# Optimization experiments

Hardware: AMD Instinct MI355X
Metric: run time of the kernel (lower is better)

Reference implementation:

```python
import jax, jax.numpy as jnp
import numpy as np

B, T, F, H = 256, 512, 64, 128


def _uniform(key, shape, stdv):
    return jax.random.uniform(key, shape, jnp.float32, -stdv, stdv)


def setup_inputs() -> dict:
    key = jax.random.key(0)
    ks = jax.random.split(key, 24)
    values = jax.random.normal(ks[0], (B, T, F), jnp.float32)
    masks = (jax.random.uniform(ks[1], (B, T, F)) < 0.8).astype(jnp.float32)
    deltas = jax.random.uniform(ks[2], (B, T, F), jnp.float32)
    labels = (jax.random.uniform(ks[3], (B, 1)) < 0.5).astype(jnp.float32)
    is_train = (jax.random.uniform(ks[4], (B, 1)) < 0.8).astype(jnp.float32)
    sH = 1.0 / np.sqrt(H)
    sF = 1.0 / np.sqrt(F)
    # temp_decay_h: Linear F -> H (stdv = 1/sqrt(out) per reset_parameters)
    W_dh = _uniform(ks[5], (H, F), sH); b_dh = _uniform(ks[6], (H,), sH)
    # temp_decay_x: diag F -> F
    W_dx = _uniform(ks[7], (F, F), sF); b_dx = _uniform(ks[8], (F,), sF)
    # hist_reg: Linear H -> F (torch Linear stdv = 1/sqrt(in))
    W_hr = _uniform(ks[9], (F, H), sH); b_hr = _uniform(ks[10], (F,), sH)
    # feat_reg: F -> F with zeroed diagonal mask
    W_fr = _uniform(ks[11], (F, F), sF); b_fr = _uniform(ks[12], (F,), sF)
    # weight_combine: Linear 2F -> F
    s2F = 1.0 / np.sqrt(2 * F)
    W_wc = _uniform(ks[13], (F, 2 * F), s2F); b_wc = _uniform(ks[14], (F,), s2F)
    # LSTMCell(2F, H): torch init uniform(-1/sqrt(H), 1/sqrt(H)), gate order i,f,g,o
    W_ih = _uniform(ks[15], (4 * H, 2 * F), sH); b_ih = _uniform(ks[16], (4 * H,), sH)
    W_hh = _uniform(ks[17], (4 * H, H), sH); b_hh = _uniform(ks[18], (4 * H,), sH)
    # out: Linear H -> 1
    W_out = _uniform(ks[19], (1, H), sH); b_out = _uniform(ks[20], (1,), sH)
    return dict(values=values, masks=masks, deltas=deltas, labels=labels, is_train=is_train,
                W_dh=W_dh, b_dh=b_dh, W_dx=W_dx, b_dx=b_dx, W_hr=W_hr, b_hr=b_hr,
                W_fr=W_fr, b_fr=b_fr, W_wc=W_wc, b_wc=b_wc,
                W_ih=W_ih, b_ih=b_ih, W_hh=W_hh, b_hh=b_hh, W_out=W_out, b_out=b_out)


def _forward(values, masks, deltas, labels, is_train,
             W_dh, b_dh, W_dx, b_dx, W_hr, b_hr, W_fr, b_fr, W_wc, b_wc,
             W_ih, b_ih, W_hh, b_hh, W_out, b_out):
    eps = 1e-5
    w_dx_diag = jnp.diagonal(W_dx)            # diag mask: W * I
    W_fr_m = W_fr * (1.0 - jnp.eye(F, dtype=W_fr.dtype))  # zero diagonal

    def step(carry, xs):
        h, c, x_loss = carry
        x, m, d = xs                           # each [B, F]
        gamma_h = jnp.exp(-jax.nn.relu(d @ W_dh.T + b_dh))   # [B, H]
        gamma_x = jnp.exp(-jax.nn.relu(d * w_dx_diag + b_dx))  # [B, F]
        h = h * gamma_h
        x_h = h @ W_hr.T + b_hr                # [B, F]
        msum = jnp.sum(m) + eps
        x_loss = x_loss + jnp.sum(jnp.abs(x - x_h) * m) / msum
        x_c = m * x + (1.0 - m) * x_h
        z_h = x_c @ W_fr_m.T + b_fr
        x_loss = x_loss + jnp.sum(jnp.abs(x - z_h) * m) / msum
        alpha = jnp.concatenate([gamma_x, m], axis=1) @ W_wc.T + b_wc
        c_h = alpha * z_h + (1.0 - alpha) * x_h
        x_loss = x_loss + jnp.sum(jnp.abs(x - c_h) * m) / msum
        c_c = m * x + (1.0 - m) * c_h
        inp = jnp.concatenate([c_c, m], axis=1)   # [B, 2F]
        gates = inp @ W_ih.T + b_ih + h @ W_hh.T + b_hh  # [B, 4H]
        i, f, g, o = jnp.split(gates, 4, axis=1)
        c = jax.nn.sigmoid(f) * c + jax.nn.sigmoid(i) * jnp.tanh(g)
        h = jax.nn.sigmoid(o) * jnp.tanh(c)
        return (h, c, x_loss), c_c

    h0 = jnp.zeros((values.shape[0], H), values.dtype)
    c0 = jnp.zeros((values.shape[0], H), values.dtype)
    xs = (jnp.swapaxes(values, 0, 1), jnp.swapaxes(masks, 0, 1), jnp.swapaxes(deltas, 0, 1))
    (h, c, x_loss), imps = jax.lax.scan(step, (h0, c0, jnp.float32(0.0)), xs)
    imputations = jnp.swapaxes(imps, 0, 1)     # [B, T, F]
    y_h = h @ W_out.T + b_out                  # [B, 1] logits
    # stable BCE with logits (matches torch reference formula)
    max_val = jnp.maximum(-y_h, 0.0)
    y_l = y_h - y_h * labels + max_val + jnp.log(jnp.exp(-max_val) + jnp.exp(-y_h - max_val))
    y_loss = jnp.sum(y_l * is_train) / (jnp.sum(is_train) + eps)
    loss = x_loss / T + y_loss * 0.3
    predictions = jax.nn.sigmoid(y_h)
    return loss, predictions, imputations


def reference(values, masks, deltas, labels, is_train,
              W_dh, b_dh, W_dx, b_dx, W_hr, b_hr, W_fr, b_fr, W_wc, b_wc,
              W_ih, b_ih, W_hh, b_hh, W_out, b_out):
    return _forward(values, masks, deltas, labels, is_train,
                    W_dh, b_dh, W_dx, b_dx, W_hr, b_hr, W_fr, b_fr, W_wc, b_wc,
                    W_ih, b_ih, W_hh, b_hh, W_out, b_out)
```

## Files before the change

### kernel.cpp

```cpp
#include <hip/hip_runtime.h>
#include <hip/hip_fp16.h>


#define NBATCH 256
#define NT 512
#define NF 64
#define NH 128

#define WHH_OFF   0u
#define WIH_OFF   131072u
#define WHR_OFF   262144u
#define WFR_OFF   278528u
#define INVMS_OFF 286720u
#define ISTR_OFF  288768u
#define GH_OFF    294912u
#define AL_OFF    33849344u

typedef _Float16 half2_t __attribute__((ext_vector_type(2)));

__device__ __forceinline__ unsigned pack2(float a, float b) {
    __half2 h = __floats2half2_rn(a, b);
    return __builtin_bit_cast(unsigned, h);
}

__device__ __forceinline__ float dot2f(unsigned w, unsigned a, float acc) {
#if __has_builtin(__builtin_amdgcn_fdot2)
    return __builtin_amdgcn_fdot2(__builtin_bit_cast(half2_t, w),
                                  __builtin_bit_cast(half2_t, a), acc, false);
#else
    float2 wf = __half22float2(__builtin_bit_cast(__half2, w));
    float2 af = __half22float2(__builtin_bit_cast(__half2, a));
    return acc + wf.x * af.x + wf.y * af.y;
#endif
}

__device__ __forceinline__ float sigm(float x) { return 1.f / (1.f + __expf(-x)); }
__device__ __forceinline__ float tanh_fast(float x) { return 1.f - 2.f / (__expf(2.f * x) + 1.f); }

__device__ __forceinline__ float quad_add_x1(float v) {
    int r = __builtin_amdgcn_update_dpp(0, __builtin_bit_cast(int, v),
                                        0xB1 , 0xF, 0xF, true);
    return v + __builtin_bit_cast(float, r);
}
__device__ __forceinline__ float quad_add_x2(float v) {
    int r = __builtin_amdgcn_update_dpp(0, __builtin_bit_cast(int, v),
                                        0x4E , 0xF, 0xF, true);
    return v + __builtin_bit_cast(float, r);
}

#define KEEP4(u) asm volatile("" : "+v"(u.x), "+v"(u.y), "+v"(u.z), "+v"(u.w))

__global__ __launch_bounds__(256) void prep_w(const float* __restrict__ Whh,
                                              const float* __restrict__ Wih,
                                              const float* __restrict__ Whr,
                                              const float* __restrict__ Wfr,
                                              unsigned* __restrict__ wsu) {
    int o = blockIdx.x * 256 + threadIdx.x;
    float v0, v1;
    if (o < 32768) {
        int c = o & 3, r = (o >> 2) & 511, cb = o >> 11;
        int col = 8 * cb + 2 * c;
        v0 = Whh[r * 128 + col]; v1 = Whh[r * 128 + col + 1];
    } else if (o < 65536) {
        int o2 = o - 32768;
        int c = o2 & 3, r = (o2 >> 2) & 511, cb = o2 >> 11;
        int col = 8 * cb + 2 * c;
        v0 = Wih[r * 128 + col]; v1 = Wih[r * 128 + col + 1];
    } else if (o < 69632) {
        int o3 = o - 65536;
        int c = o3 & 3, f = (o3 >> 2) & 63, cb = o3 >> 8;
        int col = 8 * cb + 2 * c;
        v0 = Whr[f * 128 + col]; v1 = Whr[f * 128 + col + 1];
    } else if (o < 71680) {
        int o4 = o - 69632;
        int c = o4 & 3, f = (o4 >> 2) & 63, cb = o4 >> 8;
        int col = 8 * cb + 2 * c;
        v0 = (col == f) ? 0.f : Wfr[f * 64 + col];
        v1 = (col + 1 == f) ? 0.f : Wfr[f * 64 + col + 1];
    } else {
        return;
    }
    wsu[o] = pack2(v0, v1);
}

__global__ __launch_bounds__(256) void prep_msum(const float* __restrict__ masks,
                                                 const float* __restrict__ is_train,
                                                 float* __restrict__ invms,
                                                 float* __restrict__ inv_istr,
                                                 float* __restrict__ d_out0) {
    __shared__ float red[256];
    int tid = threadIdx.x;
    int t = blockIdx.x;
    if (t < NT) {
        int f = tid & 63, br = tid >> 6;
        float s = 0.f;
        for (int i = 0; i < 64; i++) {
            int b = br + i * 4;
            s += masks[((size_t)b * NT + t) * NF + f];
        }
        red[tid] = s;
        __syncthreads();
        for (int off = 128; off > 0; off >>= 1) {
            if (tid < off) red[tid] += red[tid + off];
            __syncthreads();
        }
        if (tid == 0) invms[t] = 1.f / (red[0] + 1e-5f);
    } else {
        red[tid] = is_train[tid];
        __syncthreads();
        for (int off = 128; off > 0; off >>= 1) {
            if (tid < off) red[tid] += red[tid + off];
            __syncthreads();
        }
        if (tid == 0) {
            *inv_istr = 1.f / (red[0] + 1e-5f);
            *d_out0 = 0.f;
        }
    }
}

__global__ __launch_bounds__(256) void ga_kernel(const float* __restrict__ deltas,
                                                 const float* __restrict__ masks,
                                                 const float* __restrict__ Wdh,
                                                 const float* __restrict__ bdh,
                                                 const float* __restrict__ Wdx,
                                                 const float* __restrict__ bdx,
                                                 const float* __restrict__ Wwc,
                                                 const float* __restrict__ bwc,
                                                 __half* __restrict__ gh_all,
                                                 __half* __restrict__ al_all) {
    __shared__ unsigned wdhpk[32 * 128];
    __shared__ unsigned wwcpk[64 * 64];
    __shared__ float sbdh[128], sbdx[64], swdx[64], sbwc[64];
    __shared__ float dbuf[64];
    __shared__ __align__(16) unsigned dpk[32], gxpk[32], mpk2[32];
    int tid = threadIdx.x;

    for (int o = tid; o < 4096; o += 256) {
        int j = o & 127, k2 = o >> 7;
        wdhpk[o] = pack2(Wdh[j * 64 + 2 * k2], Wdh[j * 64 + 2 * k2 + 1]);
    }
    for (int o = tid; o < 4096; o += 256) {
        int f = o & 63, k2 = o >> 6;
        wwcpk[o] = pack2(Wwc[f * 128 + 2 * k2], Wwc[f * 128 + 2 * k2 + 1]);
    }
    if (tid < 128) sbdh[tid] = bdh[tid];
    if (tid < 64) {
        sbdx[tid] = bdx[tid];
        swdx[tid] = Wdx[tid * 65];
        sbwc[tid] = bwc[tid];
    }
    __syncthreads();

    for (int i = 0; i < 32; i++) {
        int p = blockIdx.x * 32 + i;
        if (tid < 32) {
            float2 dv = ((const float2*)(deltas + (size_t)p * NF))[tid];
            dbuf[2 * tid] = dv.x; dbuf[2 * tid + 1] = dv.y;
            dpk[tid] = pack2(dv.x, dv.y);
        } else if (tid < 64) {
            int q = tid - 32;
            float2 mv = ((const float2*)(masks + (size_t)p * NF))[q];
            mpk2[q] = pack2(mv.x, mv.y);
        }
        __syncthreads();
        if (tid < 64) {
            float gx = __expf(-fmaxf(dbuf[tid] * swdx[tid] + sbdx[tid], 0.f));
            float oth = __shfl_xor(gx, 1);
            if (!(tid & 1)) gxpk[tid >> 1] = pack2(gx, oth);
        }
        __syncthreads();
        if (tid < 128) {
            float a0 = sbdh[tid], a1 = 0.f;
            #pragma unroll
            for (int k8 = 0; k8 < 8; k8++) {
                uint4 dp = *(const uint4*)&dpk[4 * k8];
                a0 = dot2f(wdhpk[(4 * k8 + 0) * 128 + tid], dp.x, a0);
                a1 = dot2f(wdhpk[(4 * k8 + 1) * 128 + tid], dp.y, a1);
                a0 = dot2f(wdhpk[(4 * k8 + 2) * 128 + tid], dp.z, a0);
                a1 = dot2f(wdhpk[(4 * k8 + 3) * 128 + tid], dp.w, a1);
            }
            gh_all[(size_t)p * NH + tid] = __float2half(__expf(-fmaxf(a0 + a1, 0.f)));
        } else if (tid < 192) {
            int f = tid - 128;
            float a0 = sbwc[f], a1 = 0.f;
            #pragma unroll
            for (int k8 = 0; k8 < 8; k8++) {
                uint4 gp = *(const uint4*)&gxpk[4 * k8];
                a0 = dot2f(wwcpk[(4 * k8 + 0) * 64 + f], gp.x, a0);
                a1 = dot2f(wwcpk[(4 * k8 + 1) * 64 + f], gp.y, a1);
                a0 = dot2f(wwcpk[(4 * k8 + 2) * 64 + f], gp.z, a0);
                a1 = dot2f(wwcpk[(4 * k8 + 3) * 64 + f], gp.w, a1);
            }
            #pragma unroll
            for (int k8 = 0; k8 < 8; k8++) {
                uint4 mp = *(const uint4*)&mpk2[4 * k8];
                a0 = dot2f(wwcpk[(32 + 4 * k8 + 0) * 64 + f], mp.x, a0);
                a1 = dot2f(wwcpk[(32 + 4 * k8 + 1) * 64 + f], mp.y, a1);
                a0 = dot2f(wwcpk[(32 + 4 * k8 + 2) * 64 + f], mp.z, a0);
                a1 = dot2f(wwcpk[(32 + 4 * k8 + 3) * 64 + f], mp.w, a1);
            }
            al_all[(size_t)p * NF + f] = __float2half(a0 + a1);
        }
        __syncthreads();
    }
}

__global__ __launch_bounds__(512, 1) void main_kernel(
    const float* __restrict__ values, const float* __restrict__ masks,
    const float* __restrict__ labels, const float* __restrict__ is_train,
    const float* __restrict__ b_hr, const float* __restrict__ b_fr,
    const float* __restrict__ b_ih, const float* __restrict__ b_hh,
    const float* __restrict__ W_out, const float* __restrict__ b_out,
    const uint4* __restrict__ whh_ws, const uint4* __restrict__ wih_ws,
    const uint4* __restrict__ whr_ws, const uint4* __restrict__ wfr_ws,
    const float* __restrict__ invms, const float* __restrict__ inv_istr,
    const __half* __restrict__ gh_all, const __half* __restrict__ al_all,
    float* __restrict__ d_out) {
    __shared__ uint4 wm[512 * 9];
    __shared__ uint4 wfr4[8 * 64];
    __shared__ float sbhr[64], sbfr[64];
    __shared__ __align__(16) __half hph[128];
    __shared__ float xp[512];
    __shared__ float xbuf4[4][64], albuf4[4][64], mbuf4[4][64];
    __shared__ __align__(16) unsigned mpk4[4][32];
    __shared__ __align__(16) __half xcph[64], ccph[64];
    __shared__ __align__(16) unsigned ghpk4[4][64];
    __shared__ float invt4[4];
    __shared__ float hfin[128];

    const int tid = threadIdx.x;
    const int b = blockIdx.x;
    const int s = tid & 3;
    const int cq = tid >> 2;
    const int kg = tid >> 6;
    const int fl = tid & 63;

    uint4 whh_q[16];
    uint4 wihc_q[8];
    float bg4[4];
    #pragma unroll
    for (int g = 0; g < 4; g++) {
        int r = g * 128 + cq;
        #pragma unroll
        for (int j = 0; j < 4; j++) whh_q[g * 4 + j] = whh_ws[(4 * s + j) * 512 + r];
        #pragma unroll
        for (int j = 0; j < 2; j++)
            wihc_q[g * 2 + j] = wih_ws[(2 * s + j) * 512 + r];
        bg4[g] = b_ih[r] + b_hh[r];
    }
    uint4 whr_pa = whr_ws[(2 * kg) * 64 + fl];
    uint4 whr_pb = whr_ws[(2 * kg + 1) * 64 + fl];
    for (int o = tid; o < 4096; o += 512) {
        int r = o & 511, c = o >> 9;
        wm[r * 9 + c] = wih_ws[(8 + c) * 512 + r];
    }
    wfr4[tid] = wfr_ws[tid];
    if (tid < 64) { sbhr[tid] = b_hr[tid]; sbfr[tid] = b_fr[tid]; }
    if (tid < 128) hph[tid] = __float2half(0.f);

    const float* vp = values + (size_t)b * NT * NF;
    const float* mp = masks + (size_t)b * NT * NF;
    const __half* alp = al_all + (size_t)b * NT * NF;
    const unsigned* ghu = (const unsigned*)(gh_all + (size_t)b * NT * NH);
    float* imp = d_out + 257 + (size_t)b * NT * NF;

    float creg = 0.f;
    float lloss = 0.f;
    float hacc4[4] = {0.f, 0.f, 0.f, 0.f};
    float macc4[4] = {0.f, 0.f, 0.f, 0.f};
    float ccb0 = 0.f, ccb1 = 0.f, ccb2 = 0.f, ccb3 = 0.f;

    float xr4[4] = {0.f, 0.f, 0.f, 0.f};
    __half ar4[4] = {};
    float ir4[4] = {0.f, 0.f, 0.f, 0.f};
    float2 mr4[4] = {};
    unsigned gr4[4] = {0u, 0u, 0u, 0u};

    if (tid >= 256 && tid < 320) {
        int q = tid - 256;
        #pragma unroll
        for (int u = 0; u < 4; u++) {
            xr4[u] = vp[u * NF + q];
            ar4[u] = alp[u * NF + q];
        }
        if (q == 0) {
            #pragma unroll
            for (int u = 0; u < 4; u++) ir4[u] = invms[u];
        }
    } else if (tid >= 320 && tid < 352) {
        int q = tid - 320;
        #pragma unroll
        for (int u = 0; u < 4; u++) mr4[u] = ((const float2*)(mp + u * NF))[q];
    } else if (tid >= 352 && tid < 416) {
        int q = tid - 352;
        #pragma unroll
        for (int u = 0; u < 4; u++) gr4[u] = ghu[(size_t)(u + 1) * 64 + q];
    }
    __syncthreads();

    const int wmr = cq * 9;

    for (int tb = 0; tb < NT; tb += 4) {
        #pragma unroll
        for (int i = 0; i < 16; i++) { KEEP4(whh_q[i]); }
        #pragma unroll
        for (int i = 0; i < 8; i++) { KEEP4(wihc_q[i]); }
        KEEP4(whr_pa); KEEP4(whr_pb);

        #pragma unroll
        for (int j = 0; j < 4; j++) {
            const int t = tb + j;
            if (j == 0) {
                if (tid >= 256 && tid < 320) {
                    int q = tid - 256;
                    #pragma unroll
                    for (int u = 0; u < 4; u++) {
                        xbuf4[u][q] = xr4[u];
                        albuf4[u][q] = __half2float(ar4[u]);
                    }
                    if (q == 0) {
                        #pragma unroll
                        for (int u = 0; u < 4; u++) invt4[u] = ir4[u];
                    }
                    #pragma unroll
                    for (int u = 0; u < 4; u++) {
                        int tn = tb + 4 + u; if (tn > NT - 1) tn = NT - 1;
                        xr4[u] = vp[tn * NF + q];
                        ar4[u] = alp[tn * NF + q];
                    }
                    if (q == 0) {
                        #pragma unroll
                        for (int u = 0; u < 4; u++) {
                            int tn = tb + 4 + u; if (tn > NT - 1) tn = NT - 1;
                            ir4[u] = invms[tn];
                        }
                    }
                } else if (tid >= 320 && tid < 352) {
                    int q = tid - 320;
                    #pragma unroll
                    for (int u = 0; u < 4; u++) {
                        mbuf4[u][2 * q] = mr4[u].x; mbuf4[u][2 * q + 1] = mr4[u].y;
                        mpk4[u][q] = pack2(mr4[u].x, mr4[u].y);
                    }
                    #pragma unroll
                    for (int u = 0; u < 4; u++) {
                        int tn = tb + 4 + u; if (tn > NT - 1) tn = NT - 1;
                        mr4[u] = ((const float2*)(mp + tn * NF))[q];
                    }
                } else if (tid >= 352 && tid < 416) {
                    int q = tid - 352;
                    #pragma unroll
                    for (int u = 0; u < 4; u++) ghpk4[u][q] = gr4[u];
                    #pragma unroll
                    for (int u = 0; u < 4; u++) {
                        int tg = tb + 5 + u; if (tg > NT - 1) tg = NT - 1;
                        gr4[u] = ghu[(size_t)tg * 64 + q];
                    }
                }
            }
            #pragma unroll
            for (int g = 0; g < 4; g++) {
                float u0 = 0.f, u1 = 0.f;
                #pragma unroll
                for (int jj = 0; jj < 4; jj++) {
                    uint4 hq = *(const uint4*)&hph[32 * s + 8 * jj];
                    uint4 w = whh_q[g * 4 + jj];
                    u0 = dot2f(w.x, hq.x, u0); u1 = dot2f(w.y, hq.y, u1);
                    u0 = dot2f(w.z, hq.z, u0); u1 = dot2f(w.w, hq.w, u1);
                }
                hacc4[g] = u0 + u1;
            }
            {
                uint4 hpa = *(const uint4*)&hph[16 * kg];
                uint4 hpb = *(const uint4*)&hph[16 * kg + 8];
                float p0, p1;
                p0 = dot2f(whr_pa.x, hpa.x, 0.f); p1 = dot2f(whr_pa.y, hpa.y, 0.f);
                p0 = dot2f(whr_pa.z, hpa.z, p0);  p1 = dot2f(whr_pa.w, hpa.w, p1);
                p0 = dot2f(whr_pb.x, hpb.x, p0);  p1 = dot2f(whr_pb.y, hpb.y, p1);
                p0 = dot2f(whr_pb.z, hpb.z, p0);  p1 = dot2f(whr_pb.w, hpb.w, p1);
                xp[tid] = p0 + p1;
            }
            __syncthreads();

            if (tid < 64) {
                __builtin_amdgcn_s_setprio(1);
                float xh = sbhr[fl];
                #pragma unroll
                for (int g8 = 0; g8 < 8; g8++) xh += xp[g8 * 64 + fl];
                float xv = xbuf4[j][fl], mv = mbuf4[j][fl];
                float av = albuf4[j][fl], it = invt4[j];
                float xc = mv * xv + (1.f - mv) * xh;
                xcph[fl] = __float2half(xc);
                float b0 = sbfr[fl], b1 = 0.f;
                #pragma unroll
                for (int k4 = 0; k4 < 8; k4++) {
                    uint4 w = wfr4[k4 * 64 + fl];
                    uint4 xq = *(const uint4*)&xcph[8 * k4];
                    b0 = dot2f(w.x, xq.x, b0); b1 = dot2f(w.y, xq.y, b1);
                    b0 = dot2f(w.z, xq.z, b0); b1 = dot2f(w.w, xq.w, b1);
                }
                float zh = b0 + b1;
                float ch = av * zh + (1.f - av) * xh;
                float cc = mv * xv + (1.f - mv) * ch;
                if (j == 0) ccb0 = cc; else if (j == 1) ccb1 = cc;
                else if (j == 2) ccb2 = cc; else ccb3 = cc;
                lloss += (fabsf(xv - xh) + fabsf(xv - zh) + fabsf(xv - ch)) * mv * it;
                ccph[fl] = __float2half(cc);
                if (j == 3) {
                    imp[(tb + 0) * NF + fl] = ccb0;
                    imp[(tb + 1) * NF + fl] = ccb1;
                    imp[(tb + 2) * NF + fl] = ccb2;
                    imp[(tb + 3) * NF + fl] = ccb3;
                }
                __builtin_amdgcn_s_setprio(0);
            } else {
                uint4 mq0 = *(const uint4*)&mpk4[j][8 * s];
                uint4 mq1 = *(const uint4*)&mpk4[j][8 * s + 4];
                #pragma unroll
                for (int g = 0; g < 4; g++) {
                    uint4 wa = wm[(g * 128 + cq) * 9 + 2 * s];
                    uint4 wb = wm[(g * 128 + cq) * 9 + 2 * s + 1];
                    float u0 = dot2f(wa.x, mq0.x, 0.f), u1 = dot2f(wa.y, mq0.y, 0.f);
                    u0 = dot2f(wa.z, mq0.z, u0); u1 = dot2f(wa.w, mq0.w, u1);
                    u0 = dot2f(wb.x, mq1.x, u0); u1 = dot2f(wb.y, mq1.y, u1);
                    u0 = dot2f(wb.z, mq1.z, u0); u1 = dot2f(wb.w, mq1.w, u1);
                    macc4[g] = u0 + u1;
                }
            }
            __syncthreads();

            {
                if (tid < 64) {
                    uint4 mq0 = *(const uint4*)&mpk4[j][8 * s];
                    uint4 mq1 = *(const uint4*)&mpk4[j][8 * s + 4];
                    #pragma unroll
                    for (int g = 0; g < 4; g++) {
                        uint4 wa = wm[(g * 128 + cq) * 9 + 2 * s];
                        uint4 wb = wm[(g * 128 + cq) * 9 + 2 * s + 1];
                        float u0 = dot2f(wa.x, mq0.x, 0.f), u1 = dot2f(wa.y, mq0.y, 0.f);
                        u0 = dot2f(wa.z, mq0.z, u0); u1 = dot2f(wa.w, mq0.w, u1);
                        u0 = dot2f(wb.x, mq1.x, u0); u1 = dot2f(wb.y, mq1.y, u1);
                        u0 = dot2f(wb.z, mq1.z, u0); u1 = dot2f(wb.w, mq1.w, u1);
                        macc4[g] = u0 + u1;
                    }
                }
                uint4 cq0 = *(const uint4*)&ccph[16 * s];
                uint4 cq1 = *(const uint4*)&ccph[16 * s + 8];
                float gate[4];
                #pragma unroll
                for (int g = 0; g < 4; g++) {
                    uint4 wa = wihc_q[g * 2], wb = wihc_q[g * 2 + 1];
                    float u0 = dot2f(wa.x, cq0.x, 0.f), u1 = dot2f(wa.y, cq0.y, 0.f);
                    u0 = dot2f(wa.z, cq0.z, u0); u1 = dot2f(wa.w, cq0.w, u1);
                    u0 = dot2f(wb.x, cq1.x, u0); u1 = dot2f(wb.y, cq1.y, u1);
                    u0 = dot2f(wb.z, cq1.z, u0); u1 = dot2f(wb.w, cq1.w, u1);
                    float v = hacc4[g] + macc4[g] + (u0 + u1);
                    v = quad_add_x1(v);
                    v = quad_add_x2(v);
                    gate[g] = v + bg4[g];
                }
                float cn = sigm(gate[1]) * creg + sigm(gate[0]) * tanh_fast(gate[2]);
                creg = cn;
                float hn = sigm(gate[3]) * tanh_fast(cn);
                float gm = __half2float(((const __half*)&ghpk4[j][0])[cq]);
                float hd = hn * gm;
                if (s == 0) hph[cq] = __float2half(hd);
                if (t == NT - 1 && s == 0) hfin[cq] = hn;
            }
            __syncthreads();
        }
    }

    if (tid < 64) {
        float ll = lloss;
        float yp = hfin[tid] * W_out[tid] + hfin[64 + tid] * W_out[64 + tid];
        #pragma unroll
        for (int off = 32; off > 0; off >>= 1) {
            ll += __shfl_down(ll, off);
            yp += __shfl_down(yp, off);
        }
        if (tid == 0) {
            float yh = yp + b_out[0];
            d_out[1 + b] = 1.f / (1.f + expf(-yh));
            float lab = labels[b], istr = is_train[b];
            float maxv = fmaxf(-yh, 0.f);
            float yl = yh - yh * lab + maxv + logf(expf(-maxv) + expf(-yh - maxv));
            atomicAdd(d_out, ll * (1.f / (float)NT) + 0.3f * yl * istr * (*inv_istr));
        }
    }
}

extern "C" void kernel_launch(void* const* d_in, const int* in_sizes, int n_in,
                              void* d_out, int out_size, void* d_ws, size_t ws_size,
                              hipStream_t stream) {
    const float* values = (const float*)d_in[0];
    const float* masks = (const float*)d_in[1];
    const float* deltas = (const float*)d_in[2];
    const float* labels = (const float*)d_in[3];
    const float* is_train = (const float*)d_in[4];
    const float* W_dh = (const float*)d_in[5];
    const float* b_dh = (const float*)d_in[6];
    const float* W_dx = (const float*)d_in[7];
    const float* b_dx = (const float*)d_in[8];
    const float* W_hr = (const float*)d_in[9];
    const float* b_hr = (const float*)d_in[10];
    const float* W_fr = (const float*)d_in[11];
    const float* b_fr = (const float*)d_in[12];
    const float* W_wc = (const float*)d_in[13];
    const float* b_wc = (const float*)d_in[14];
    const float* W_ih = (const float*)d_in[15];
    const float* b_ih = (const float*)d_in[16];
    const float* W_hh = (const float*)d_in[17];
    const float* b_hh = (const float*)d_in[18];
    const float* W_out = (const float*)d_in[19];
    const float* b_out = (const float*)d_in[20];

    char* ws = (char*)d_ws;
    unsigned* wsu = (unsigned*)d_ws;
    const uint4* whh_ws = (const uint4*)(ws + WHH_OFF);
    const uint4* wih_ws = (const uint4*)(ws + WIH_OFF);
    const uint4* whr_ws = (const uint4*)(ws + WHR_OFF);
    const uint4* wfr_ws = (const uint4*)(ws + WFR_OFF);
    float* invms = (float*)(ws + INVMS_OFF);
    float* inv_istr = (float*)(ws + ISTR_OFF);
    __half* gh_all = (__half*)(ws + GH_OFF);
    __half* al_all = (__half*)(ws + AL_OFF);
    float* out_f = (float*)d_out;

    prep_w<<<280, 256, 0, stream>>>(W_hh, W_ih, W_hr, W_fr, wsu);
    prep_msum<<<513, 256, 0, stream>>>(masks, is_train, invms, inv_istr, out_f);
    ga_kernel<<<4096, 256, 0, stream>>>(deltas, masks, W_dh, b_dh, W_dx, b_dx,
                                        W_wc, b_wc, gh_all, al_all);
    main_kernel<<<NBATCH, 512, 0, stream>>>(values, masks, labels, is_train,
                                            b_hr, b_fr, b_ih, b_hh, W_out, b_out,
                                            whh_ws, wih_ws, whr_ws, wfr_ws,
                                            invms, inv_istr, gh_all, al_all, out_f);
}
```

Baseline: 1.240 ms.

## Precompute mask-input LSTM gate contributions in parallel pre-pass kernel

Moves the W_ih·mask term of the LSTM gates (plus the biases) out of the sequential main kernel into the parallel ga_kernel. There it is written as a half-precision gate tensor that main_kernel prefetches per timestep. This takes dot products off the recurrent critical path and frees one LDS weight block. In exchange it adds about 128 MB of extra global writes and reads, and the path only runs when the workspace is large enough.

```diff
diff --git a/kernel.cpp b/kernel.cpp
--- a/kernel.cpp
+++ b/kernel.cpp
@@ -15,6 +15,8 @@
 #define ISTR_OFF  288768u
 #define GH_OFF    294912u
 #define AL_OFF    33849344u
+#define GM4_OFF   50626560u
+#define GM4_BYTES 134217728u
 
 typedef _Float16 half2_t __attribute__((ext_vector_type(2)));
 
@@ -127,8 +129,13 @@
                                                  const float* __restrict__ bdx,
                                                  const float* __restrict__ Wwc,
                                                  const float* __restrict__ bwc,
+                                                 const float* __restrict__ bih,
+                                                 const float* __restrict__ bhh,
+                                                 const uint4* __restrict__ wih_ws,
                                                  __half* __restrict__ gh_all,
-                                                 __half* __restrict__ al_all) {
+                                                 __half* __restrict__ al_all,
+                                                 __half* __restrict__ gm4_all,
+                                                 int do_gm) {
     __shared__ unsigned wdhpk[32 * 128];
     __shared__ unsigned wwcpk[64 * 64];
     __shared__ float sbdh[128], sbdx[64], swdx[64], sbwc[64];
@@ -149,6 +156,17 @@
         sbdx[tid] = bdx[tid];
         swdx[tid] = Wdx[tid * 65];
         sbwc[tid] = bwc[tid];
+    }
+    uint4 wmr0[8], wmr1[8];
+    float bgr0 = 0.f, bgr1 = 0.f;
+    if (do_gm) {
+        #pragma unroll
+        for (int c = 0; c < 8; c++) {
+            wmr0[c] = wih_ws[(8 + c) * 512 + tid];
+            wmr1[c] = wih_ws[(8 + c) * 512 + tid + 256];
+        }
+        bgr0 = bih[tid] + bhh[tid];
+        bgr1 = bih[tid + 256] + bhh[tid + 256];
     }
     __syncthreads();
 
@@ -202,6 +220,21 @@
             }
             al_all[(size_t)p * NF + f] = __float2half(a0 + a1);
         }
+        if (do_gm) {
+            float a0 = bgr0, a1 = 0.f, b0 = bgr1, b1 = 0.f;
+            #pragma unroll
+            for (int k8 = 0; k8 < 8; k8++) {
+                uint4 mp = *(const uint4*)&mpk2[4 * k8];
+                a0 = dot2f(wmr0[k8].x, mp.x, a0); a1 = dot2f(wmr0[k8].y, mp.y, a1);
+                a0 = dot2f(wmr0[k8].z, mp.z, a0); a1 = dot2f(wmr0[k8].w, mp.w, a1);
+                b0 = dot2f(wmr1[k8].x, mp.x, b0); b1 = dot2f(wmr1[k8].y, mp.y, b1);
+                b0 = dot2f(wmr1[k8].z, mp.z, b0); b1 = dot2f(wmr1[k8].w, mp.w, b1);
+            }
+            int cell = tid & 127;
+            int g0 = tid >> 7;
+            gm4_all[(size_t)p * 512 + cell * 4 + g0] = __float2half(a0 + a1);
+            gm4_all[(size_t)p * 512 + cell * 4 + g0 + 2] = __float2half(b0 + b1);
+        }
         __syncthreads();
     }
 }
@@ -216,6 +249,7 @@
     const uint4* __restrict__ whr_ws, const uint4* __restrict__ wfr_ws,
     const float* __restrict__ invms, const float* __restrict__ inv_istr,
     const __half* __restrict__ gh_all, const __half* __restrict__ al_all,
+    const __half* __restrict__ gm4_all,
     float* __restrict__ d_out) {
     __shared__ uint4 wm[512 * 9];
     __shared__ uint4 wfr4[8 * 64];
@@ -235,6 +269,7 @@
     const int cq = tid >> 2;
     const int kg = tid >> 6;
     const int fl = tid & 63;
+    const bool use_gm = (gm4_all != nullptr);
 
     uint4 whh_q[16];
     uint4 wihc_q[8];
@@ -251,9 +286,11 @@
     }
     uint4 whr_pa = whr_ws[(2 * kg) * 64 + fl];
     uint4 whr_pb = whr_ws[(2 * kg + 1) * 64 + fl];
-    for (int o = tid; o < 4096; o += 512) {
-        int r = o & 511, c = o >> 9;
-        wm[r * 9 + c] = wih_ws[(8 + c) * 512 + r];
+    if (!use_gm) {
+        for (int o = tid; o < 4096; o += 512) {
+            int r = o & 511, c = o >> 9;
+            wm[r * 9 + c] = wih_ws[(8 + c) * 512 + r];
+        }
     }
     wfr4[tid] = wfr_ws[tid];
     if (tid < 64) { sbhr[tid] = b_hr[tid]; sbfr[tid] = b_fr[tid]; }
@@ -263,6 +300,7 @@
     const float* mp = masks + (size_t)b * NT * NF;
     const __half* alp = al_all + (size_t)b * NT * NF;
     const unsigned* ghu = (const unsigned*)(gh_all + (size_t)b * NT * NH);
+    const __half* gmp = use_gm ? (gm4_all + (size_t)b * NT * 512) : nullptr;
     float* imp = d_out + 257 + (size_t)b * NT * NF;
 
     float creg = 0.f;
@@ -276,6 +314,7 @@
     float ir4[4] = {0.f, 0.f, 0.f, 0.f};
     float2 mr4[4] = {};
     unsigned gr4[4] = {0u, 0u, 0u, 0u};
+    uint2 gmr4[4] = {}; uint2 gmc[4] = {};
 
     if (tid >= 256 && tid < 320) {
         int q = tid - 256;
@@ -297,9 +336,12 @@
         #pragma unroll
         for (int u = 0; u < 4; u++) gr4[u] = ghu[(size_t)(u + 1) * 64 + q];
     }
+    if (use_gm) {
+        #pragma unroll
+        for (int u = 0; u < 4; u++)
+            gmr4[u] = *(const uint2*)(gmp + (size_t)u * 512 + cq * 4);
+    }
     __syncthreads();
-
-    const int wmr = cq * 9;
 
     for (int tb = 0; tb < NT; tb += 4) {
         #pragma unroll
@@ -341,7 +383,7 @@
                     #pragma unroll
                     for (int u = 0; u < 4; u++) {
                         mbuf4[u][2 * q] = mr4[u].x; mbuf4[u][2 * q + 1] = mr4[u].y;
-                        mpk4[u][q] = pack2(mr4[u].x, mr4[u].y);
+                        if (!use_gm) mpk4[u][q] = pack2(mr4[u].x, mr4[u].y);
                     }
                     #pragma unroll
                     for (int u = 0; u < 4; u++) {
@@ -356,6 +398,15 @@
                     for (int u = 0; u < 4; u++) {
                         int tg = tb + 5 + u; if (tg > NT - 1) tg = NT - 1;
                         gr4[u] = ghu[(size_t)tg * 64 + q];
+                    }
+                }
+                if (use_gm) {
+                    #pragma unroll
+                    for (int u = 0; u < 4; u++) gmc[u] = gmr4[u];
+                    #pragma unroll
+                    for (int u = 0; u < 4; u++) {
+                        int tn = tb + 4 + u; if (tn > NT - 1) tn = NT - 1;
+                        gmr4[u] = *(const uint2*)(gmp + (size_t)tn * 512 + cq * 4);
                     }
                 }
             }
@@ -414,7 +465,7 @@
                     imp[(tb + 3) * NF + fl] = ccb3;
                 }
                 __builtin_amdgcn_s_setprio(0);
-            } else {
+            } else if (!use_gm) {
                 uint4 mq0 = *(const uint4*)&mpk4[j][8 * s];
                 uint4 mq1 = *(const uint4*)&mpk4[j][8 * s + 4];
                 #pragma unroll
@@ -431,7 +482,7 @@
             __syncthreads();
 
             {
-                if (tid < 64) {
+                if (!use_gm && tid < 64) {
                     uint4 mq0 = *(const uint4*)&mpk4[j][8 * s];
                     uint4 mq1 = *(const uint4*)&mpk4[j][8 * s + 4];
                     #pragma unroll
@@ -444,6 +495,12 @@
                         u0 = dot2f(wb.z, mq1.z, u0); u1 = dot2f(wb.w, mq1.w, u1);
                         macc4[g] = u0 + u1;
                     }
+                }
+                float gmf[4] = {bg4[0], bg4[1], bg4[2], bg4[3]};
+                if (use_gm) {
+                    float2 f01 = __half22float2(__builtin_bit_cast(__half2, gmc[j].x));
+                    float2 f23 = __half22float2(__builtin_bit_cast(__half2, gmc[j].y));
+                    gmf[0] = f01.x; gmf[1] = f01.y; gmf[2] = f23.x; gmf[3] = f23.y;
                 }
                 uint4 cq0 = *(const uint4*)&ccph[16 * s];
                 uint4 cq1 = *(const uint4*)&ccph[16 * s + 8];
@@ -455,10 +512,11 @@
                     u0 = dot2f(wa.z, cq0.z, u0); u1 = dot2f(wa.w, cq0.w, u1);
                     u0 = dot2f(wb.x, cq1.x, u0); u1 = dot2f(wb.y, cq1.y, u1);
                     u0 = dot2f(wb.z, cq1.z, u0); u1 = dot2f(wb.w, cq1.w, u1);
-                    float v = hacc4[g] + macc4[g] + (u0 + u1);
+                    float v = hacc4[g] + (u0 + u1);
+                    if (!use_gm) v += macc4[g];
                     v = quad_add_x1(v);
                     v = quad_add_x2(v);
-                    gate[g] = v + bg4[g];
+                    gate[g] = v + gmf[g];
                 }
                 float cn = sigm(gate[1]) * creg + sigm(gate[0]) * tanh_fast(gate[2]);
                 creg = cn;
@@ -526,14 +584,18 @@
     float* inv_istr = (float*)(ws + ISTR_OFF);
     __half* gh_all = (__half*)(ws + GH_OFF);
     __half* al_all = (__half*)(ws + AL_OFF);
+    const int do_gm = (ws_size >= (size_t)GM4_OFF + (size_t)GM4_BYTES) ? 1 : 0;
+    __half* gm4_all = do_gm ? (__half*)(ws + GM4_OFF) : nullptr;
     float* out_f = (float*)d_out;
 
     prep_w<<<280, 256, 0, stream>>>(W_hh, W_ih, W_hr, W_fr, wsu);
     prep_msum<<<513, 256, 0, stream>>>(masks, is_train, invms, inv_istr, out_f);
     ga_kernel<<<4096, 256, 0, stream>>>(deltas, masks, W_dh, b_dh, W_dx, b_dx,
-                                        W_wc, b_wc, gh_all, al_all);
+                                        W_wc, b_wc, b_ih, b_hh, wih_ws,
+                                        gh_all, al_all, gm4_all, do_gm);
     main_kernel<<<NBATCH, 512, 0, stream>>>(values, masks, labels, is_train,
                                             b_hr, b_fr, b_ih, b_hh, W_out, b_out,
                                             whh_ws, wih_ws, whr_ws, wfr_ws,
-                                            invms, inv_istr, gh_all, al_all, out_f);
-}
+                                            invms, inv_istr, gh_all, al_all,
+                                            gm4_all, out_f);
+}
```

New measurement: 1.293 ms. +4.2%, slower.
